# Kernel tuning notes

Measured on AMD Instinct MI355X. Metric: run time of the kernel, lower is better.

## Reference

```python
import jax, jax.numpy as jnp
import numpy as np

N = 100000
E = 3200000
NFEAT = 512
NHID = 256


def setup_inputs() -> dict:
    key = jax.random.key(0)
    ks = jax.random.split(key, 8)
    x = jax.random.normal(ks[0], (N, NFEAT), dtype=jnp.float32)
    edge_row = jax.random.randint(ks[1], (E,), 0, N, dtype=jnp.int32)
    edge_col = jax.random.randint(ks[2], (E,), 0, N, dtype=jnp.int32)
    edge_val = jax.random.uniform(ks[3], (E,), dtype=jnp.float32)
    # xavier_uniform init as in reset_parameters
    lim1 = np.sqrt(6.0 / (NFEAT + NHID)).astype(np.float32)
    lim2 = np.sqrt(6.0 / (NHID + NHID)).astype(np.float32)
    W1 = jax.random.uniform(ks[4], (NFEAT, NHID), minval=-lim1, maxval=lim1, dtype=jnp.float32)
    W2 = jax.random.uniform(ks[5], (NHID, NHID), minval=-lim2, maxval=lim2, dtype=jnp.float32)
    b1 = jnp.zeros((NHID,), dtype=jnp.float32)
    b2 = jnp.zeros((NHID,), dtype=jnp.float32)
    alpha = jnp.full((1,), 0.25, dtype=jnp.float32)  # PReLU single weight
    return {"x": x, "edge_row": edge_row, "edge_col": edge_col,
            "edge_val": edge_val, "W1": W1, "b1": b1, "W2": W2, "b2": b2,
            "alpha": alpha}


def _spmm(edge_row, edge_col, edge_val, support):
    # out[i] = sum over edges e with row[e]==i of val[e] * support[col[e]]
    msgs = support[edge_col] * edge_val[:, None]  # [E, F]
    return jax.ops.segment_sum(msgs, edge_row, num_segments=N)


def _prelu(x, alpha):
    return jnp.where(x >= 0, x, alpha * x)


def reference(x, edge_row, edge_col, edge_val, W1, b1, W2, b2, alpha):
    # Layer 1: GraphConvolution(nfeat, nhid) -> PReLU (dropout=0 -> identity)
    h = _spmm(edge_row, edge_col, edge_val, x @ W1) + b1
    h = _prelu(h, alpha)
    # Layer 2: GraphConvolution(nhid, nhid) -> PReLU
    h = _spmm(edge_row, edge_col, edge_val, h @ W2) + b2
    h = _prelu(h, alpha)
    return h
```

## Files before the change

kernel.cpp:

```cpp
#include <hip/hip_runtime.h>

#define NHID 256
#define BSHIFT 6
#define BROWS  (1 << BSHIFT)

typedef __attribute__((ext_vector_type(8))) short short8;
typedef __attribute__((ext_vector_type(4))) float floatx4;
typedef __attribute__((ext_vector_type(4))) float float4v;
typedef __attribute__((ext_vector_type(4))) int int4v;
typedef __attribute__((ext_vector_type(4))) unsigned int uint4v;

static __device__ __forceinline__ short f2bf(float f) {
    unsigned u = __float_as_uint(f);
    unsigned r = (u + 0x7fffu + ((u >> 16) & 1u)) >> 16;
    return (short)r;
}
static __device__ __forceinline__ unsigned pk2(float a, float b) {
    return ((unsigned)(unsigned short)f2bf(a)) | (((unsigned)(unsigned short)f2bf(b)) << 16);
}

__global__ void transpose_cast2(const float* __restrict__ W1, short* __restrict__ W1t,
                                const float* __restrict__ W2, short* __restrict__ W2t,
                                int K1, int K2)
{
    int idx = blockIdx.x * 256 + threadIdx.x;
    int n1 = K1 * NHID;
    if (idx < n1) {
        int k = idx >> 8;
        int n = idx & 255;
        W1t[(size_t)n * K1 + k] = f2bf(W1[idx]);
    } else {
        int j = idx - n1;
        if (j < K2 * NHID) {
            int k = j >> 8;
            int n = j & 255;
            W2t[(size_t)n * K2 + k] = f2bf(W2[j]);
        }
    }
}

template<bool ABF16>
__global__ __launch_bounds__(512) void gemm_mfma(
    const void* __restrict__ Ap, const short* __restrict__ Bt,
    short* __restrict__ C, int M, int K)
{
    __shared__ __align__(16) short As[128][40];
    __shared__ __align__(16) short Bs[256][40];

    int tid  = threadIdx.x;
    int m0   = blockIdx.x * 128;
    int lane = tid & 63;
    int wid  = tid >> 6;
    int wm   = wid >> 2;
    int wn   = wid & 3;
    int quad = lane >> 4;
    int l16  = lane & 15;

    floatx4 acc[4][4] = {};

    for (int k0 = 0; k0 < K; k0 += 32) {
        if (ABF16) {
            const short* A = (const short*)Ap;
            int tr = tid >> 2, tc = (tid & 3) * 8;
            int gm = m0 + tr;
            int4v v = {0, 0, 0, 0};
            if (gm < M) v = __builtin_nontemporal_load((const int4v*)(A + (size_t)gm * K + k0 + tc));
            *(int4v*)&As[tr][tc] = v;
        } else {
            const float* A = (const float*)Ap;
            int tr = tid >> 3, tc = (tid & 7) * 4;
            #pragma unroll
            for (int p = 0; p < 2; ++p) {
                int m = p * 64 + tr, gm = m0 + m;
                float4v v = {0.f, 0.f, 0.f, 0.f};
                if (gm < M) v = __builtin_nontemporal_load((const float4v*)(A + (size_t)gm * K + k0 + tc));
                short4 s;
                s.x = f2bf(v.x); s.y = f2bf(v.y); s.z = f2bf(v.z); s.w = f2bf(v.w);
                *(short4*)&As[m][tc] = s;
            }
        }
        {
            int nr = tid >> 2, nc = (tid & 3) * 8;
            #pragma unroll
            for (int p = 0; p < 2; ++p) {
                int n = p * 128 + nr;
                *(int4*)&Bs[n][nc] = *(const int4*)(Bt + (size_t)n * K + k0 + nc);
            }
        }
        __syncthreads();

        short8 af[4], bfr[4];
        #pragma unroll
        for (int t = 0; t < 4; ++t) {
            af[t]  = *(const short8*)&As[wm * 64 + t * 16 + l16][quad * 8];
            bfr[t] = *(const short8*)&Bs[wn * 64 + t * 16 + l16][quad * 8];
        }
        #pragma unroll
        for (int tm = 0; tm < 4; ++tm)
            #pragma unroll
            for (int tn = 0; tn < 4; ++tn)
                acc[tm][tn] = __builtin_amdgcn_mfma_f32_16x16x32_bf16(
                    af[tm], bfr[tn], acc[tm][tn], 0, 0, 0);
        __syncthreads();
    }

    #pragma unroll
    for (int tm = 0; tm < 4; ++tm) {
        #pragma unroll
        for (int r = 0; r < 4; ++r) {
            int row = m0 + wm * 64 + tm * 16 + quad * 4 + r;
            if (row < M) {
                #pragma unroll
                for (int tn = 0; tn < 4; ++tn) {
                    int col = wn * 64 + tn * 16 + l16;
                    C[(size_t)row * NHID + col] = f2bf(acc[tm][tn][r]);
                }
            }
        }
    }
}

__global__ void hist_kernel(const int* __restrict__ rows, int* __restrict__ counts, int E)
{
    int i = blockIdx.x * blockDim.x + threadIdx.x;
    if (i < E) atomicAdd(&counts[rows[i]], 1);
}

__global__ __launch_bounds__(256) void block_scan(
    const int* __restrict__ counts, int* __restrict__ tmp, int* __restrict__ bsum, int n)
{
    __shared__ int ws[4];
    int tid = threadIdx.x, b = blockIdx.x;
    int i = b * 256 + tid;
    int lane = tid & 63, w = tid >> 6;
    int v = (i < n) ? counts[i] : 0;
    int x = v;
    #pragma unroll
    for (int off = 1; off < 64; off <<= 1) {
        int y = __shfl_up(x, off, 64);
        if (lane >= off) x += y;
    }
    if (lane == 63) ws[w] = x;
    __syncthreads();
    int add = 0;
    #pragma unroll
    for (int k = 0; k < 4; ++k) if (k < w) add += ws[k];
    x += add;
    if (i < n) tmp[i] = x;
    if (tid == 255) bsum[b] = x;
}

__global__ __launch_bounds__(256) void scan_bsums(int* __restrict__ bsum, int nb)
{
    __shared__ int ws[4];
    __shared__ int carry;
    int tid = threadIdx.x, lane = tid & 63, w = tid >> 6;
    if (tid == 0) carry = 0;
    __syncthreads();
    for (int base = 0; base < nb; base += 256) {
        int i = base + tid;
        int v = (i < nb) ? bsum[i] : 0;
        int x = v;
        #pragma unroll
        for (int off = 1; off < 64; off <<= 1) {
            int y = __shfl_up(x, off, 64);
            if (lane >= off) x += y;
        }
        if (lane == 63) ws[w] = x;
        __syncthreads();
        int add = 0;
        #pragma unroll
        for (int k = 0; k < 4; ++k) if (k < w) add += ws[k];
        int incl = x + add;
        int c = carry;
        if (i < nb) bsum[i] = incl - v + c;
        __syncthreads();
        if (tid == 255) carry = c + incl;
        __syncthreads();
    }
}

__global__ void finalize_scan(const int* __restrict__ tmp, const int* __restrict__ boff,
                              int* __restrict__ row_ptr, int n)
{
    int i = blockIdx.x * 256 + threadIdx.x;
    if (i < n) row_ptr[i + 1] = tmp[i] + boff[i >> 8];
    if (i == 0) row_ptr[0] = 0;
}

__global__ void bucket_stage(
    const int* __restrict__ erow, const int* __restrict__ ecol,
    const float* __restrict__ eval, const int* __restrict__ row_ptr,
    int* __restrict__ bcur, int2* __restrict__ stage, int E)
{
    int i = blockIdx.x * 256 + threadIdx.x;
    if (i >= E) return;
    int r = erow[i];
    int b = r >> BSHIFT;
    int base = row_ptr[b << BSHIFT];
    int pos = base + atomicAdd(&bcur[b * 16], 1);
    stage[pos] = make_int2(ecol[i] | ((r & (BROWS - 1)) << 20), __float_as_int(eval[i]));
}

__global__ __launch_bounds__(256) void bucket_place(
    const int* __restrict__ row_ptr, const int2* __restrict__ stage,
    int2* __restrict__ ep, int N)
{
    __shared__ int lfill[BROWS];
    int b  = blockIdx.x;
    int r0 = b << BSHIFT;
    int r1 = min(N, r0 + BROWS);
    if (threadIdx.x < BROWS) lfill[threadIdx.x] = 0;
    __syncthreads();
    int base = row_ptr[r0];
    int end  = row_ptr[r1];
    for (int i = base + threadIdx.x; i < end; i += 256) {
        int2 sv = stage[i];
        int rl  = ((unsigned)sv.x) >> 20;
        int col = sv.x & 0xFFFFF;
        int slot = row_ptr[r0 + rl] + atomicAdd(&lfill[rl], 1);
        ep[slot] = make_int2(col, sv.y);
    }
}

static __device__ __forceinline__ void fma8(float* acc, uint4 g, float v)
{
    acc[0] += v * __uint_as_float(g.x << 16);
    acc[1] += v * __uint_as_float(g.x & 0xffff0000u);
    acc[2] += v * __uint_as_float(g.y << 16);
    acc[3] += v * __uint_as_float(g.y & 0xffff0000u);
    acc[4] += v * __uint_as_float(g.z << 16);
    acc[5] += v * __uint_as_float(g.z & 0xffff0000u);
    acc[6] += v * __uint_as_float(g.w << 16);
    acc[7] += v * __uint_as_float(g.w & 0xffff0000u);
}

template<bool OUT_BF16>
__global__ __launch_bounds__(256) void spmm_split(
    const int* __restrict__ row_ptr, const int2* __restrict__ ep,
    const short* __restrict__ dense,
    const float* __restrict__ bias, const float* __restrict__ alpha_p,
    void* __restrict__ outp, int nrows)
{
    int wid  = (blockIdx.x * blockDim.x + threadIdx.x) >> 6;
    int lane = threadIdx.x & 63;
    if (wid >= nrows) return;
    int half = lane >> 5;
    int l32  = lane & 31;
    int s = row_ptr[wid], e = row_ptr[wid + 1];
    int fo = l32 * 8;

    float acc[8] = {};
    int i = s;
    for (; i + 3 < e; i += 4) {
        int2 e0 = ep[i + half];
        int2 e1 = ep[i + 2 + half];
        uint4 g0 = *(const uint4*)(dense + (size_t)e0.x * NHID + fo);
        uint4 g1 = *(const uint4*)(dense + (size_t)e1.x * NHID + fo);
        fma8(acc, g0, __int_as_float(e0.y));
        fma8(acc, g1, __int_as_float(e1.y));
    }
    for (; i < e; i += 2) {
        int j = i + half;
        if (j < e) {
            int2 e0 = ep[j];
            uint4 g0 = *(const uint4*)(dense + (size_t)e0.x * NHID + fo);
            fma8(acc, g0, __int_as_float(e0.y));
        }
    }

    #pragma unroll
    for (int k = 0; k < 8; ++k) acc[k] += __shfl_xor(acc[k], 32, 64);

    float alpha = alpha_p[0];
    float4 b0 = *(const float4*)(bias + fo);
    float4 b1 = *(const float4*)(bias + fo + 4);
    float r[8];
    r[0] = acc[0] + b0.x; r[1] = acc[1] + b0.y; r[2] = acc[2] + b0.z; r[3] = acc[3] + b0.w;
    r[4] = acc[4] + b1.x; r[5] = acc[5] + b1.y; r[6] = acc[6] + b1.z; r[7] = acc[7] + b1.w;
    #pragma unroll
    for (int k = 0; k < 8; ++k) r[k] = (r[k] >= 0.f) ? r[k] : alpha * r[k];

    if (OUT_BF16) {
        if (half == 0) {
            uint4 o;
            o.x = pk2(r[0], r[1]); o.y = pk2(r[2], r[3]);
            o.z = pk2(r[4], r[5]); o.w = pk2(r[6], r[7]);
            *(uint4*)((short*)outp + (size_t)wid * NHID + fo) = o;
        }
    } else {
        float4v ov;
        if (half) { ov.x = r[4]; ov.y = r[5]; ov.z = r[6]; ov.w = r[7]; }
        else      { ov.x = r[0]; ov.y = r[1]; ov.z = r[2]; ov.w = r[3]; }
        __builtin_nontemporal_store(ov, (float4v*)((float*)outp + (size_t)wid * NHID + fo + half * 4));
    }
}

extern "C" void kernel_launch(void* const* d_in, const int* in_sizes, int n_in,
                              void* d_out, int out_size, void* d_ws, size_t ws_size,
                              hipStream_t stream)
{
    const float* x     = (const float*)d_in[0];
    const int*   erow  = (const int*)d_in[1];
    const int*   ecol  = (const int*)d_in[2];
    const float* eval  = (const float*)d_in[3];
    const float* W1    = (const float*)d_in[4];
    const float* b1    = (const float*)d_in[5];
    const float* W2    = (const float*)d_in[6];
    const float* b2    = (const float*)d_in[7];
    const float* alpha = (const float*)d_in[8];

    int NFEAT = 512;
    int N = in_sizes[0] / NFEAT;
    int E = in_sizes[1];
    float* out = (float*)d_out;

    char* wsp = (char*)d_ws;
    short* support_b = (short*)wsp;  wsp += (size_t)N * NHID * sizeof(short);
    short* h1b       = (short*)wsp;  wsp += (size_t)N * NHID * sizeof(short);
    int2*  ep        = (int2*)wsp;   wsp += (size_t)E * sizeof(int2);
    int*   row_ptr   = (int*)wsp;    wsp += ((size_t)(N + 1) * sizeof(int) + 15) & ~(size_t)15;
    short* W1t       = (short*)wsp;  wsp += (size_t)NFEAT * NHID * sizeof(short);
    short* W2t       = (short*)wsp;  wsp += (size_t)NHID * NHID * sizeof(short);

    int NB   = (N + BROWS - 1) >> BSHIFT;
    int nblk = (N + 255) / 256;

    int* counts = (int*)h1b;
    int* bcur   = counts + N;
    int* tmp    = bcur + (size_t)NB * 16;
    int* bsum   = tmp + N;

    int2* stage = (int2*)support_b;

    transpose_cast2<<<((NFEAT + NHID) * NHID + 255) / 256, 256, 0, stream>>>(
        W1, W1t, W2, W2t, NFEAT, NHID);

    hipMemsetAsync(counts, 0, ((size_t)N + (size_t)NB * 16) * sizeof(int), stream);
    hist_kernel<<<(E + 255) / 256, 256, 0, stream>>>(erow, counts, E);
    block_scan<<<nblk, 256, 0, stream>>>(counts, tmp, bsum, N);
    scan_bsums<<<1, 256, 0, stream>>>(bsum, nblk);
    finalize_scan<<<nblk, 256, 0, stream>>>(tmp, bsum, row_ptr, N);
    bucket_stage<<<(E + 255) / 256, 256, 0, stream>>>(erow, ecol, eval, row_ptr, bcur, stage, E);
    bucket_place<<<NB, 256, 0, stream>>>(row_ptr, stage, ep, N);

    int ggrid = (N + 127) / 128;
    int spmm_blocks = (N + 3) / 4;

    gemm_mfma<false><<<ggrid, 512, 0, stream>>>(x, W1t, support_b, N, NFEAT);
    spmm_split<true><<<spmm_blocks, 256, 0, stream>>>(row_ptr, ep, support_b, b1, alpha, h1b, N);
    gemm_mfma<true><<<ggrid, 512, 0, stream>>>(h1b, W2t, support_b, N, NHID);
    spmm_split<false><<<spmm_blocks, 256, 0, stream>>>(row_ptr, ep, support_b, b2, alpha, out, N);
}
```

Baseline: 1.156 ms.

## Rebuild CSR construction with partitioned bucket keys and in-block row_ptr

Replaces the per-row histogram plus multi-kernel scan with a histogram over (row-bucket, partition) keys, where the partition comes from the block index. A single 1024-thread block scans these keys, and edges are staged by atomic increments on the spread-out key counters. A placement kernel then counts rows within each bucket in shared memory, writes row_ptr itself and scatters the edges. This is meant to cut kernel launches and the global atomic contention on each bucket counter, at the cost of a serial single-block scan over about 12.5K keys.

```diff
diff --git a/kernel.cpp b/kernel.cpp
--- a/kernel.cpp
+++ b/kernel.cpp
@@ -3,6 +3,7 @@
 #define NHID 256
 #define BSHIFT 6
 #define BROWS  (1 << BSHIFT)
+#define NPART  8
 
 typedef __attribute__((ext_vector_type(8))) short short8;
 typedef __attribute__((ext_vector_type(4))) float floatx4;
@@ -120,46 +121,27 @@
     }
 }
 
-__global__ void hist_kernel(const int* __restrict__ rows, int* __restrict__ counts, int E)
-{
-    int i = blockIdx.x * blockDim.x + threadIdx.x;
-    if (i < E) atomicAdd(&counts[rows[i]], 1);
-}
-
-__global__ __launch_bounds__(256) void block_scan(
-    const int* __restrict__ counts, int* __restrict__ tmp, int* __restrict__ bsum, int n)
-{
-    __shared__ int ws[4];
-    int tid = threadIdx.x, b = blockIdx.x;
-    int i = b * 256 + tid;
-    int lane = tid & 63, w = tid >> 6;
-    int v = (i < n) ? counts[i] : 0;
-    int x = v;
-    #pragma unroll
-    for (int off = 1; off < 64; off <<= 1) {
-        int y = __shfl_up(x, off, 64);
-        if (lane >= off) x += y;
-    }
-    if (lane == 63) ws[w] = x;
+
+__global__ void key_hist(const int* __restrict__ erow, int* __restrict__ keycnt, int E)
+{
+    int i = blockIdx.x * 256 + threadIdx.x;
+    if (i >= E) return;
+    int key = ((erow[i] >> BSHIFT) << 3) | (blockIdx.x & (NPART - 1));
+    atomicAdd(&keycnt[key], 1);
+}
+
+__global__ __launch_bounds__(1024) void key_scan(
+    const int* __restrict__ keycnt, int* __restrict__ keybase,
+    int* __restrict__ bucket_start, int nkey, int nb, int E)
+{
+    __shared__ int ws[16];
+    __shared__ int carry_s;
+    int tid = threadIdx.x, lane = tid & 63, w = tid >> 6;
+    if (tid == 0) carry_s = 0;
     __syncthreads();
-    int add = 0;
-    #pragma unroll
-    for (int k = 0; k < 4; ++k) if (k < w) add += ws[k];
-    x += add;
-    if (i < n) tmp[i] = x;
-    if (tid == 255) bsum[b] = x;
-}
-
-__global__ __launch_bounds__(256) void scan_bsums(int* __restrict__ bsum, int nb)
-{
-    __shared__ int ws[4];
-    __shared__ int carry;
-    int tid = threadIdx.x, lane = tid & 63, w = tid >> 6;
-    if (tid == 0) carry = 0;
-    __syncthreads();
-    for (int base = 0; base < nb; base += 256) {
+    for (int base = 0; base < nkey; base += 1024) {
         int i = base + tid;
-        int v = (i < nb) ? bsum[i] : 0;
+        int v = (i < nkey) ? keycnt[i] : 0;
         int x = v;
         #pragma unroll
         for (int off = 1; off < 64; off <<= 1) {
@@ -168,59 +150,82 @@
         }
         if (lane == 63) ws[w] = x;
         __syncthreads();
-        int add = 0;
-        #pragma unroll
-        for (int k = 0; k < 4; ++k) if (k < w) add += ws[k];
+        if (w == 0 && lane < 16) {
+            int s = ws[lane];
+            #pragma unroll
+            for (int off = 1; off < 16; off <<= 1) {
+                int y = __shfl_up(s, off, 16);
+                if (lane >= off) s += y;
+            }
+            ws[lane] = s;
+        }
+        __syncthreads();
+        int add = (w > 0) ? ws[w - 1] : 0;
         int incl = x + add;
-        int c = carry;
-        if (i < nb) bsum[i] = incl - v + c;
-        __syncthreads();
-        if (tid == 255) carry = c + incl;
-        __syncthreads();
-    }
-}
-
-__global__ void finalize_scan(const int* __restrict__ tmp, const int* __restrict__ boff,
-                              int* __restrict__ row_ptr, int n)
-{
-    int i = blockIdx.x * 256 + threadIdx.x;
-    if (i < n) row_ptr[i + 1] = tmp[i] + boff[i >> 8];
-    if (i == 0) row_ptr[0] = 0;
-}
-
-__global__ void bucket_stage(
+        int c = carry_s;
+        int excl = incl - v + c;
+        if (i < nkey) {
+            keybase[i] = excl;
+            if ((i & (NPART - 1)) == 0) bucket_start[i >> 3] = excl;
+        }
+        __syncthreads();
+        if (tid == 1023) carry_s = c + incl;
+        __syncthreads();
+    }
+    if (tid == 0) bucket_start[nb] = E;
+}
+
+__global__ void stage_part(
     const int* __restrict__ erow, const int* __restrict__ ecol,
-    const float* __restrict__ eval, const int* __restrict__ row_ptr,
-    int* __restrict__ bcur, int2* __restrict__ stage, int E)
+    const float* __restrict__ eval,
+    int* __restrict__ keycur, int2* __restrict__ staged, int E)
 {
     int i = blockIdx.x * 256 + threadIdx.x;
     if (i >= E) return;
     int r = erow[i];
-    int b = r >> BSHIFT;
-    int base = row_ptr[b << BSHIFT];
-    int pos = base + atomicAdd(&bcur[b * 16], 1);
-    stage[pos] = make_int2(ecol[i] | ((r & (BROWS - 1)) << 20), __float_as_int(eval[i]));
-}
-
-__global__ __launch_bounds__(256) void bucket_place(
-    const int* __restrict__ row_ptr, const int2* __restrict__ stage,
-    int2* __restrict__ ep, int N)
-{
-    __shared__ int lfill[BROWS];
+    int key = ((r >> BSHIFT) << 3) | (blockIdx.x & (NPART - 1));
+    int pos = atomicAdd(&keycur[key], 1);
+    staged[pos] = make_int2(ecol[i] | ((r & (BROWS - 1)) << 20), __float_as_int(eval[i]));
+}
+
+__global__ __launch_bounds__(256) void place_rowptr(
+    const int* __restrict__ bucket_start, const int2* __restrict__ staged,
+    int2* __restrict__ ep, int* __restrict__ row_ptr, int N, int E)
+{
+    __shared__ int rcnt[BROWS];
+    __shared__ int rbase[BROWS];
     int b  = blockIdx.x;
     int r0 = b << BSHIFT;
-    int r1 = min(N, r0 + BROWS);
-    if (threadIdx.x < BROWS) lfill[threadIdx.x] = 0;
+    int nr = min(N - r0, BROWS);
+    int s = bucket_start[b], e = bucket_start[b + 1];
+    if (threadIdx.x < BROWS) rcnt[threadIdx.x] = 0;
     __syncthreads();
-    int base = row_ptr[r0];
-    int end  = row_ptr[r1];
-    for (int i = base + threadIdx.x; i < end; i += 256) {
-        int2 sv = stage[i];
-        int rl  = ((unsigned)sv.x) >> 20;
-        int col = sv.x & 0xFFFFF;
-        int slot = row_ptr[r0 + rl] + atomicAdd(&lfill[rl], 1);
-        ep[slot] = make_int2(col, sv.y);
-    }
+    for (int i = s + threadIdx.x; i < e; i += 256) {
+        int rl = ((unsigned)staged[i].x) >> 20;
+        atomicAdd(&rcnt[rl], 1);
+    }
+    __syncthreads();
+    if (threadIdx.x < BROWS) {
+        int v = rcnt[threadIdx.x];
+        int x = v;
+        #pragma unroll
+        for (int off = 1; off < 64; off <<= 1) {
+            int y = __shfl_up(x, off, 64);
+            if (threadIdx.x >= off) x += y;
+        }
+        int excl = s + x - v;
+        rbase[threadIdx.x] = excl;
+        if (threadIdx.x < nr) row_ptr[r0 + threadIdx.x] = excl;
+        rcnt[threadIdx.x] = 0;
+    }
+    __syncthreads();
+    for (int i = s + threadIdx.x; i < e; i += 256) {
+        int2 sv = staged[i];
+        int rl = ((unsigned)sv.x) >> 20;
+        int slot = rbase[rl] + atomicAdd(&rcnt[rl], 1);
+        ep[slot] = make_int2(sv.x & 0xFFFFF, sv.y);
+    }
+    if (b == gridDim.x - 1 && threadIdx.x == 0) row_ptr[N] = E;
 }
 
 static __device__ __forceinline__ void fma8(float* acc, uint4 g, float v)
@@ -324,25 +329,23 @@
     short* W2t       = (short*)wsp;  wsp += (size_t)NHID * NHID * sizeof(short);
 
     int NB   = (N + BROWS - 1) >> BSHIFT;
-    int nblk = (N + 255) / 256;
-
-    int* counts = (int*)h1b;
-    int* bcur   = counts + N;
-    int* tmp    = bcur + (size_t)NB * 16;
-    int* bsum   = tmp + N;
-
-    int2* stage = (int2*)support_b;
+    int NKEY = NB * NPART;
+
+    int* keycnt       = (int*)h1b;
+    int* keybase      = keycnt + NKEY;
+    int* bucket_start = keybase + NKEY;
+
+    int2* staged = (int2*)support_b;
 
     transpose_cast2<<<((NFEAT + NHID) * NHID + 255) / 256, 256, 0, stream>>>(
         W1, W1t, W2, W2t, NFEAT, NHID);
 
-    hipMemsetAsync(counts, 0, ((size_t)N + (size_t)NB * 16) * sizeof(int), stream);
-    hist_kernel<<<(E + 255) / 256, 256, 0, stream>>>(erow, counts, E);
-    block_scan<<<nblk, 256, 0, stream>>>(counts, tmp, bsum, N);
-    scan_bsums<<<1, 256, 0, stream>>>(bsum, nblk);
-    finalize_scan<<<nblk, 256, 0, stream>>>(tmp, bsum, row_ptr, N);
-    bucket_stage<<<(E + 255) / 256, 256, 0, stream>>>(erow, ecol, eval, row_ptr, bcur, stage, E);
-    bucket_place<<<NB, 256, 0, stream>>>(row_ptr, stage, ep, N);
+    hipMemsetAsync(keycnt, 0, (size_t)NKEY * sizeof(int), stream);
+    int egrid = (E + 255) / 256;
+    key_hist<<<egrid, 256, 0, stream>>>(erow, keycnt, E);
+    key_scan<<<1, 1024, 0, stream>>>(keycnt, keybase, bucket_start, NKEY, NB, E);
+    stage_part<<<egrid, 256, 0, stream>>>(erow, ecol, eval, keybase, staged, E);
+    place_rowptr<<<NB, 256, 0, stream>>>(bucket_start, staged, ep, row_ptr, N, E);
 
     int ggrid = (N + 127) / 128;
     int spmm_blocks = (N + 3) / 4;
```

After: 1.172 ms. About the same (+1.4%).
